# Kernel tuning notes

Hardware: AMD Instinct MI355X
Metric: run time of the kernel (lower is better)

## Reference

```python
import jax, jax.numpy as jnp
import numpy as np

B, C_IN, H, W = 32, 128, 64, 64
C_OUT, K, STRIDE, PAD = 128, 3, 1, 1
M, G = 2, 2
RC = max(C_IN // 16, 16)          # reduction channels = 16
MO = M * C_OUT                    # 256
GRP = G * C_OUT                   # fc groups = 256
OPG = (C_OUT * C_IN * K * K) // GRP   # 576 outputs per fc group
IPG = MO // GRP                   # 1 input per fc group
EPS = 1e-5


def setup_inputs() -> dict:
    key = jax.random.key(0)
    ks = jax.random.split(key, 12)
    s = 0.02
    return {
        "x": jax.random.normal(ks[0], (B, C_IN, H, W), jnp.float32),
        "mask_w": jax.random.normal(ks[1], (1, C_IN), jnp.float32) * s,
        "mask_b": jnp.zeros((1,), jnp.float32),
        "t1_w": jax.random.normal(ks[2], (RC, C_IN), jnp.float32) * s,
        "t1_b": jnp.zeros((RC,), jnp.float32),
        "ln_g": jnp.ones((RC,), jnp.float32),
        "ln_b": jnp.zeros((RC,), jnp.float32),
        "t2_w": jax.random.normal(ks[3], (MO, RC), jnp.float32) * s,
        "t2_b": jnp.zeros((MO,), jnp.float32),
        "fc_w": jax.random.normal(ks[4], (GRP, OPG, IPG), jnp.float32) * s,
        "fc_b": jnp.zeros((GRP * OPG,), jnp.float32),
    }


def reference(x, mask_w, mask_b, t1_w, t1_b, ln_g, ln_b, t2_w, t2_b, fc_w, fc_b):
    b, c, h, w = x.shape
    # --- GC attention context pooling ---
    logits = jnp.einsum('bchw,oc->bohw', x, mask_w) + mask_b[None, :, None, None]
    attn = jax.nn.softmax(logits.reshape(b, h * w), axis=-1)  # [b, hw]
    context = jnp.einsum('bchw,bs->bc', x, attn.reshape(b, h * w)) if False else \
        jnp.einsum('bcs,bs->bc', x.reshape(b, c, h * w), attn)
    # --- transform: conv1x1 -> LayerNorm -> ReLU -> conv1x1 ---
    t = jnp.einsum('bc,rc->br', context, t1_w) + t1_b
    mu = jnp.mean(t, axis=-1, keepdims=True)
    var = jnp.mean((t - mu) ** 2, axis=-1, keepdims=True)
    t = (t - mu) * jax.lax.rsqrt(var + EPS) * ln_g + ln_b
    t = jax.nn.relu(t)
    xw = jnp.einsum('br,or->bo', t, t2_w) + t2_b          # [b, M*out]
    xw = jax.nn.sigmoid(xw)
    # --- grouped 1x1 fc: generates per-sample conv weights ---
    xg = xw.reshape(b, GRP, IPG)
    gen = jnp.einsum('goi,bgi->bgo', fc_w, xg) + fc_b.reshape(GRP, OPG)
    w_gen = gen.reshape(b, C_OUT, C_IN, K, K)             # per-sample kernels
    # --- per-sample conv (groups=b trick in torch) ---
    def conv_one(xi, wi):
        return jax.lax.conv_general_dilated(
            xi[None], wi, (STRIDE, STRIDE), [(PAD, PAD), (PAD, PAD)],
            dimension_numbers=('NCHW', 'OIHW', 'NCHW'))[0]
    out = jax.vmap(conv_one)(x, w_gen)                    # [b, out, h, w]
    return out
```

## Files before the change

kernel.cpp:

```cpp
#include <hip/hip_runtime.h>
#include <hip/hip_bf16.h>

typedef unsigned short u16;
typedef unsigned int u32;
typedef __attribute__((ext_vector_type(8))) short bf16x8;
typedef __attribute__((ext_vector_type(16))) float f32x16;
typedef __attribute__((ext_vector_type(4))) int int4v;
typedef __attribute__((ext_vector_type(4))) float f32x4;

#define CIN 128
#define COUT 128
#define HWSZ 4096
#define RC 16
#define EPS 1e-5f

__device__ __forceinline__ float b2f(u16 u) {
    u32 v = ((u32)u) << 16;
    union { u32 i; float f; } c; c.i = v; return c.f;
}

__device__ __forceinline__ void dma16(const void* g, void* l) {
    __builtin_amdgcn_global_load_lds((const __attribute__((address_space(1))) void*)g,
                                     (__attribute__((address_space(3))) void*)l, 16, 0, 0);
}

__global__ __launch_bounds__(256) void k_xform(const float* __restrict__ x,
                                               const float* __restrict__ mask_w,
                                               const float* __restrict__ mask_b,
                                               u16* __restrict__ xT,
                                               float* __restrict__ attn,
                                               float* __restrict__ sumexp) {
    int y = blockIdx.x, b = blockIdx.y, t = threadIdx.x;
    __shared__ float tile[128 * 65];
    __shared__ float red[256];

    int c4 = t & 15, ci0 = t >> 4;
#pragma unroll
    for (int i = 0; i < 8; ++i) {
        int ci = ci0 + i * 16;
        f32x4 v = *(const f32x4*)(x + (size_t)(b * 128 + ci) * 4096 + y * 64 + c4 * 4);
        float* tr = tile + ci * 65 + c4 * 4;
        tr[0] = v.x; tr[1] = v.y; tr[2] = v.z; tr[3] = v.w;
    }
    __syncthreads();

    {
        int xs = t & 63, grp = t >> 6;
        float a = 0.f;
#pragma unroll 8
        for (int ci = grp * 32; ci < grp * 32 + 32; ++ci)
            a = fmaf(tile[ci * 65 + xs], mask_w[ci], a);
        red[grp * 64 + xs] = a;
    }

    {
        int xs = t >> 2, q = t & 3;
        u16* dst = xT + ((size_t)b * 4096 + y * 64 + xs) * 128;
        int sw = xs & 7;
#pragma unroll
        for (int k = 0; k < 4; ++k) {
            int cd = q * 4 + k;
            int cs = cd ^ sw;
            u16 tmp[8];
#pragma unroll
            for (int e = 0; e < 8; ++e) {
                __hip_bfloat16 h = __float2bfloat16(tile[(cd * 8 + e) * 65 + xs]);
                tmp[e] = *reinterpret_cast<u16*>(&h);
            }
            *(int4v*)(dst + cs * 8) = *(int4v*)tmp;
        }
    }
    __syncthreads();
    if (t < 64) {
        float e = __expf(red[t] + red[64 + t] + red[128 + t] + red[192 + t] + mask_b[0]);
        attn[b * HWSZ + y * 64 + t] = e;
        float s = e;
#pragma unroll
        for (int off = 32; off; off >>= 1) s += __shfl_down(s, off);
        if (t == 0) atomicAdd(&sumexp[b], s);
    }
}

__global__ __launch_bounds__(256) void k_context(const u16* __restrict__ xT,
                                                 const float* __restrict__ attn,
                                                 const float* __restrict__ sumexp,
                                                 float* __restrict__ ctx) {
    int bid = blockIdx.x;
    int b = bid >> 4, sc = bid & 15;
    int t = threadIdx.x;
    int px = t >> 4, cg = t & 15;
    const char* xb = (const char*)(xT + (size_t)b * HWSZ * 128);
    float acc[8] = {0.f, 0.f, 0.f, 0.f, 0.f, 0.f, 0.f, 0.f};
    int s0 = sc * 256 + px;
    int coff = (cg * 16) ^ ((px & 7) << 4);
    for (int j = 0; j < 16; ++j) {
        int s = s0 + j * 16;
        float e = attn[b * HWSZ + s];
        int4v u = *(const int4v*)(xb + (size_t)s * 256 + coff);
        const u16* q = (const u16*)&u;
#pragma unroll
        for (int k = 0; k < 8; ++k) acc[k] = fmaf(e, b2f(q[k]), acc[k]);
    }
    __shared__ float red[16][132];
#pragma unroll
    for (int k = 0; k < 8; ++k) red[px][cg * 8 + k] = acc[k];
    __syncthreads();
    if (t < 128) {
        float s = 0.f;
#pragma unroll
        for (int g = 0; g < 16; ++g) s += red[g][t];
        atomicAdd(&ctx[b * 128 + t], s / sumexp[b]);
    }
}

__global__ __launch_bounds__(256) void k_genw(const float* __restrict__ ctx,
                                              const float* __restrict__ t1_w,
                                              const float* __restrict__ t1_b,
                                              const float* __restrict__ ln_g,
                                              const float* __restrict__ ln_b,
                                              const float* __restrict__ t2_w,
                                              const float* __restrict__ t2_b,
                                              const float* __restrict__ fc_w,
                                              const float* __restrict__ fc_b,
                                              u16* __restrict__ wgen) {
    int bid = blockIdx.x;
    int b = bid >> 3, g = bid & 7;
    int t = threadIdx.x;
    __shared__ float ctx_sh[128];
    __shared__ float traw[RC];
    __shared__ float gate_sh[64];
    if (t < 128) ctx_sh[t] = ctx[b * 128 + t];
    __syncthreads();
    if (t < RC) {
        float a = 0.f;
        for (int c = 0; c < 128; ++c) a = fmaf(ctx_sh[c], t1_w[t * 128 + c], a);
        traw[t] = a + t1_b[t];
    }
    __syncthreads();
    int r32g = g >> 1;
    if (t < 64) {
        float tv[RC], mu = 0.f;
#pragma unroll
        for (int r = 0; r < RC; ++r) { tv[r] = traw[r]; mu += tv[r]; }
        mu *= (1.f / RC);
        float var = 0.f;
#pragma unroll
        for (int r = 0; r < RC; ++r) { float d = tv[r] - mu; var = fmaf(d, d, var); }
        var *= (1.f / RC);
        float rs = rsqrtf(var + EPS);
        int gi = r32g * 64 + t;
        float xw = 0.f;
#pragma unroll
        for (int r = 0; r < RC; ++r) {
            float a = fmaxf(0.f, fmaf((tv[r] - mu) * rs, ln_g[r], ln_b[r]));
            xw = fmaf(a, t2_w[gi * RC + r], xw);
        }
        xw += t2_b[gi];
        gate_sh[t] = 1.f / (1.f + __expf(-xw));
    }
    __syncthreads();
    int U = g * 256 + t;
    int r32 = U >> 9, c = (U >> 5) & 15, l31 = U & 31;
    int co = r32 * 32 + l31;
    float gate = gate_sh[l31 * 2 + (c >> 3)];
    int base = co * 1152 + c * 72;
    float wv[72], bv[72];
#pragma unroll
    for (int i = 0; i < 18; ++i) {
        *(f32x4*)&wv[i * 4] = *(const f32x4*)(fc_w + base + i * 4);
        *(f32x4*)&bv[i * 4] = *(const f32x4*)(fc_b + base + i * 4);
    }
    u16* wb = wgen + (size_t)b * 9 * 16384;
    int unit = r32 * 512 + c * 32 + l31;
#pragma unroll
    for (int p = 0; p < 9; ++p) {
        u16 tmp[8];
#pragma unroll
        for (int e = 0; e < 8; ++e) {
            float v = fmaf(wv[e * 9 + p], gate, bv[e * 9 + p]);
            __hip_bfloat16 h = __float2bfloat16(v);
            tmp[e] = *reinterpret_cast<u16*>(&h);
        }
        *(int4v*)(wb + p * 16384 + unit * 8) = *(int4v*)tmp;
    }
}

__global__ __launch_bounds__(256, 2) void k_conv(const u16* __restrict__ xT,
                                                 const u16* __restrict__ wgen,
                                                 float* __restrict__ out) {
    __shared__ __align__(16) u16 Bt[132 * 128];

    int bid0 = blockIdx.x;
    int xcd = bid0 & 7, i5 = bid0 >> 3;
    int b = xcd * 4 + (i5 >> 5);
    int yp = i5 & 31, y0 = yp * 2;

    int t = threadIdx.x;
    int lane = t & 63, w = t >> 6;
    int wr = w >> 1, wc = w & 1;
    int l31 = lane & 31, l5 = lane >> 5;

    const char* xb = (const char*)(xT + (size_t)b * HWSZ * 128);
    const char* wbase = (const char*)(wgen + (size_t)b * 9 * 16384);
    const char* abase = wbase + wr * 16384 + l5 * 512 + l31 * 16;

    bf16x8 RA[16], RB[16];
    f32x16 acc00 = {0}, acc01 = {0}, acc10 = {0}, acc11 = {0};
    const char* Bb = (const char*)Bt;
    int rowB0 = wc * 66 + l31;

#define LOADP(P, R)                                                        \
    {                                                                      \
        const char* ap = abase + (P) * 32768;                              \
        _Pragma("unroll") for (int ks = 0; ks < 8; ++ks) {                 \
            R[ks]     = *(const bf16x8*)(ap + ks * 1024);                  \
            R[8 + ks] = *(const bf16x8*)(ap + 8192 + ks * 1024);           \
        }                                                                  \
    }

#define COMPUTE(P, R)                                                              \
    {                                                                              \
        const int kw = (P) % 3;                                                    \
        int rB0 = (rowB0 + kw) << 8;                                               \
        int rB1 = rB0 + (32 << 8);                                                 \
        int sB = ((l31 + kw - 1) & 7) << 4;                                        \
        _Pragma("unroll") for (int ks = 0; ks < 8; ++ks) {                         \
            int kb = ks * 32 + l5 * 16;                                            \
            bf16x8 b0 = *(const bf16x8*)(Bb + (rB0 | (kb ^ sB)));                  \
            bf16x8 b1 = *(const bf16x8*)(Bb + (rB1 | (kb ^ sB)));                  \
            acc00 = __builtin_amdgcn_mfma_f32_32x32x16_bf16(R[ks], b0, acc00, 0, 0, 0);     \
            acc01 = __builtin_amdgcn_mfma_f32_32x32x16_bf16(R[ks], b1, acc01, 0, 0, 0);     \
            acc10 = __builtin_amdgcn_mfma_f32_32x32x16_bf16(R[8 + ks], b0, acc10, 0, 0, 0); \
            acc11 = __builtin_amdgcn_mfma_f32_32x32x16_bf16(R[8 + ks], b1, acc11, 0, 0, 0); \
        }                                                                          \
    }

#define STAGEB(KH)                                                                   \
    {                                                                                \
        _Pragma("unroll") for (int r = 0; r < 2; ++r) {                              \
            int y = y0 + r + (KH) - 1;                                               \
            char* base = (char*)Bt + (r * 66) * 256;                                 \
            if ((unsigned)y < 64u) {                                                 \
                const char* src = xb + (size_t)y * 64 * 256;                         \
                _Pragma("unroll") for (int i = 0; i < 4; ++i) {                      \
                    int off = (w * 4 + i) * 1024;                                    \
                    dma16(src + off + lane * 16, base + 256 + off);                  \
                }                                                                    \
                if (t < 32) {                                                        \
                    int hr = (t >> 4) * 65;                                          \
                    *(int4v*)(base + hr * 256 + (t & 15) * 16) = int4v{0, 0, 0, 0};  \
                }                                                                    \
            } else {                                                                 \
                for (int i = t; i < 1056; i += 256)                                  \
                    *(int4v*)(base + i * 16) = int4v{0, 0, 0, 0};                    \
            }                                                                        \
        }                                                                            \
    }

    LOADP(0, RA);
#pragma unroll
    for (int p = 0; p < 9; ++p) {
        if (p % 3 == 0) {
            __syncthreads();
            STAGEB(p / 3);
            __syncthreads();
        }
        if (p < 8) {
            if (p & 1) { LOADP(p + 1, RA); } else { LOADP(p + 1, RB); }
        }
        if (p & 1) { COMPUTE(p, RB); } else { COMPUTE(p, RA); }
    }

    float* ob = out + (size_t)b * COUT * HWSZ;
    int y = y0 + wc;
    auto store_acc = [&](const f32x16& v, int m2, int n4) {
        float* colp = ob + (size_t)(wr * 64 + m2 * 32) * HWSZ + y * 64 + n4 * 32 + l31;
#pragma unroll
        for (int r = 0; r < 16; ++r) {
            int row32 = (r & 3) + ((r >> 2) << 3) + (l5 << 2);
            colp[(size_t)row32 * HWSZ] = v[r];
        }
    };
    store_acc(acc00, 0, 0);
    store_acc(acc01, 0, 1);
    store_acc(acc10, 1, 0);
    store_acc(acc11, 1, 1);
#undef LOADP
#undef COMPUTE
#undef STAGEB
}

extern "C" void kernel_launch(void* const* d_in, const int* in_sizes, int n_in,
                              void* d_out, int out_size, void* d_ws, size_t ws_size,
                              hipStream_t stream) {
    const float* x      = (const float*)d_in[0];
    const float* mask_w = (const float*)d_in[1];
    const float* mask_b = (const float*)d_in[2];
    const float* t1_w   = (const float*)d_in[3];
    const float* t1_b   = (const float*)d_in[4];
    const float* ln_g   = (const float*)d_in[5];
    const float* ln_b   = (const float*)d_in[6];
    const float* t2_w   = (const float*)d_in[7];
    const float* t2_b   = (const float*)d_in[8];
    const float* fc_w   = (const float*)d_in[9];
    const float* fc_b   = (const float*)d_in[10];
    float* out = (float*)d_out;

    char* ws = (char*)d_ws;
    u16*   xT     = (u16*)ws;
    float* attn   = (float*)(ws + 33554432);
    float* ctx    = (float*)(ws + 34078720);
    float* sumexp = (float*)(ws + 34095104);
    u16*   wgen   = (u16*)(ws + 34096128);

    hipMemsetAsync(ws + 34078720, 0, 17408, stream);

    k_xform  <<<dim3(64, 32), 256, 0, stream>>>(x, mask_w, mask_b, xT, attn, sumexp);
    k_context<<<512, 256, 0, stream>>>(xT, attn, sumexp, ctx);
    k_genw   <<<256, 256, 0, stream>>>(ctx, t1_w, t1_b, ln_g, ln_b,
                                       t2_w, t2_b, fc_w, fc_b, wgen);
    k_conv   <<<1024, 256, 0, stream>>>(xT, wgen, out);
}
```

Baseline: 215.5 us.

## Fuse context pooling into transform kernel, re-grid weight generation, stage conv rows once

The attention-weighted context sum moves into k_xform. Each block computes unnormalized exp weights per row and accumulates e*x into the context buffer with atomics. This removes the separate k_context kernel and the attn buffer round trip. k_genw is re-gridded to 2048 blocks, with each thread producing one (co,ci) pair and writing scalar bf16 stores, and normalization by sumexp is deferred to it. k_conv stages all four input rows into LDS once up front instead of three synchronized restaging phases. This doubles its LDS use and may reduce occupancy.

Result: faster. 209.9 us (-2.6%).

```diff
diff --git a/kernel.cpp b/kernel.cpp
--- a/kernel.cpp
+++ b/kernel.cpp
@@ -14,11 +14,6 @@
 #define RC 16
 #define EPS 1e-5f
 
-__device__ __forceinline__ float b2f(u16 u) {
-    u32 v = ((u32)u) << 16;
-    union { u32 i; float f; } c; c.i = v; return c.f;
-}
-
 __device__ __forceinline__ void dma16(const void* g, void* l) {
     __builtin_amdgcn_global_load_lds((const __attribute__((address_space(1))) void*)g,
                                      (__attribute__((address_space(3))) void*)l, 16, 0, 0);
@@ -28,19 +23,19 @@
                                                const float* __restrict__ mask_w,
                                                const float* __restrict__ mask_b,
                                                u16* __restrict__ xT,
-                                               float* __restrict__ attn,
+                                               float* __restrict__ ctxU,
                                                float* __restrict__ sumexp) {
     int y = blockIdx.x, b = blockIdx.y, t = threadIdx.x;
-    __shared__ float tile[128 * 65];
+    __shared__ float tile[128 * 68];
     __shared__ float red[256];
+    __shared__ float e_sh[64];
 
     int c4 = t & 15, ci0 = t >> 4;
 #pragma unroll
     for (int i = 0; i < 8; ++i) {
         int ci = ci0 + i * 16;
         f32x4 v = *(const f32x4*)(x + (size_t)(b * 128 + ci) * 4096 + y * 64 + c4 * 4);
-        float* tr = tile + ci * 65 + c4 * 4;
-        tr[0] = v.x; tr[1] = v.y; tr[2] = v.z; tr[3] = v.w;
+        *(f32x4*)(tile + ci * 68 + c4 * 4) = v;
     }
     __syncthreads();
 
@@ -49,9 +44,19 @@
         float a = 0.f;
 #pragma unroll 8
         for (int ci = grp * 32; ci < grp * 32 + 32; ++ci)
-            a = fmaf(tile[ci * 65 + xs], mask_w[ci], a);
-        red[grp * 64 + xs] = a;
-    }
+            a = fmaf(tile[ci * 68 + xs], mask_w[ci], a);
+        red[t] = a;
+    }
+    __syncthreads();
+    if (t < 64) {
+        float e = __expf(red[t] + red[64 + t] + red[128 + t] + red[192 + t] + mask_b[0]);
+        e_sh[t] = e;
+        float s = e;
+#pragma unroll
+        for (int off = 32; off; off >>= 1) s += __shfl_down(s, off);
+        if (t == 0) atomicAdd(&sumexp[b], s);
+    }
+    __syncthreads();
 
     {
         int xs = t >> 2, q = t & 3;
@@ -63,57 +68,29 @@
             int cs = cd ^ sw;
             u16 tmp[8];
 #pragma unroll
-            for (int e = 0; e < 8; ++e) {
-                __hip_bfloat16 h = __float2bfloat16(tile[(cd * 8 + e) * 65 + xs]);
-                tmp[e] = *reinterpret_cast<u16*>(&h);
+            for (int e2 = 0; e2 < 8; ++e2) {
+                __hip_bfloat16 h = __float2bfloat16(tile[(cd * 8 + e2) * 68 + xs]);
+                tmp[e2] = *reinterpret_cast<u16*>(&h);
             }
             *(int4v*)(dst + cs * 8) = *(int4v*)tmp;
         }
     }
-    __syncthreads();
-    if (t < 64) {
-        float e = __expf(red[t] + red[64 + t] + red[128 + t] + red[192 + t] + mask_b[0]);
-        attn[b * HWSZ + y * 64 + t] = e;
-        float s = e;
-#pragma unroll
-        for (int off = 32; off; off >>= 1) s += __shfl_down(s, off);
-        if (t == 0) atomicAdd(&sumexp[b], s);
-    }
-}
-
-__global__ __launch_bounds__(256) void k_context(const u16* __restrict__ xT,
-                                                 const float* __restrict__ attn,
-                                                 const float* __restrict__ sumexp,
-                                                 float* __restrict__ ctx) {
-    int bid = blockIdx.x;
-    int b = bid >> 4, sc = bid & 15;
-    int t = threadIdx.x;
-    int px = t >> 4, cg = t & 15;
-    const char* xb = (const char*)(xT + (size_t)b * HWSZ * 128);
-    float acc[8] = {0.f, 0.f, 0.f, 0.f, 0.f, 0.f, 0.f, 0.f};
-    int s0 = sc * 256 + px;
-    int coff = (cg * 16) ^ ((px & 7) << 4);
-    for (int j = 0; j < 16; ++j) {
-        int s = s0 + j * 16;
-        float e = attn[b * HWSZ + s];
-        int4v u = *(const int4v*)(xb + (size_t)s * 256 + coff);
-        const u16* q = (const u16*)&u;
-#pragma unroll
-        for (int k = 0; k < 8; ++k) acc[k] = fmaf(e, b2f(q[k]), acc[k]);
-    }
-    __shared__ float red[16][132];
-#pragma unroll
-    for (int k = 0; k < 8; ++k) red[px][cg * 8 + k] = acc[k];
-    __syncthreads();
-    if (t < 128) {
-        float s = 0.f;
-#pragma unroll
-        for (int g = 0; g < 16; ++g) s += red[g][t];
-        atomicAdd(&ctx[b * 128 + t], s / sumexp[b]);
-    }
-}
-
-__global__ __launch_bounds__(256) void k_genw(const float* __restrict__ ctx,
+
+    {
+        int ci = t >> 1, half = t & 1;
+        float a = 0.f;
+#pragma unroll
+        for (int j = 0; j < 32; ++j) {
+            int xs = half * 32 + j;
+            a = fmaf(tile[ci * 68 + xs], e_sh[xs], a);
+        }
+        a += __shfl_xor(a, 1);
+        if (half == 0) atomicAdd(&ctxU[b * 128 + ci], a);
+    }
+}
+
+__global__ __launch_bounds__(256) void k_genw(const float* __restrict__ ctxU,
+                                              const float* __restrict__ sumexp,
                                               const float* __restrict__ t1_w,
                                               const float* __restrict__ t1_b,
                                               const float* __restrict__ ln_g,
@@ -124,12 +101,12 @@
                                               const float* __restrict__ fc_b,
                                               u16* __restrict__ wgen) {
     int bid = blockIdx.x;
-    int b = bid >> 3, g = bid & 7;
+    int b = bid >> 6, c64 = bid & 63;
     int t = threadIdx.x;
     __shared__ float ctx_sh[128];
     __shared__ float traw[RC];
-    __shared__ float gate_sh[64];
-    if (t < 128) ctx_sh[t] = ctx[b * 128 + t];
+    __shared__ float gate_sh[4];
+    if (t < 128) ctx_sh[t] = ctxU[b * 128 + t] / sumexp[b];
     __syncthreads();
     if (t < RC) {
         float a = 0.f;
@@ -137,8 +114,7 @@
         traw[t] = a + t1_b[t];
     }
     __syncthreads();
-    int r32g = g >> 1;
-    if (t < 64) {
+    if (t < 4) {
         float tv[RC], mu = 0.f;
 #pragma unroll
         for (int r = 0; r < RC; ++r) { tv[r] = traw[r]; mu += tv[r]; }
@@ -148,7 +124,7 @@
         for (int r = 0; r < RC; ++r) { float d = tv[r] - mu; var = fmaf(d, d, var); }
         var *= (1.f / RC);
         float rs = rsqrtf(var + EPS);
-        int gi = r32g * 64 + t;
+        int gi = (c64 * 2 + (t >> 1)) * 2 + (t & 1);
         float xw = 0.f;
 #pragma unroll
         for (int r = 0; r < RC; ++r) {
@@ -159,36 +135,26 @@
         gate_sh[t] = 1.f / (1.f + __expf(-xw));
     }
     __syncthreads();
-    int U = g * 256 + t;
-    int r32 = U >> 9, c = (U >> 5) & 15, l31 = U & 31;
-    int co = r32 * 32 + l31;
-    float gate = gate_sh[l31 * 2 + (c >> 3)];
-    int base = co * 1152 + c * 72;
-    float wv[72], bv[72];
-#pragma unroll
-    for (int i = 0; i < 18; ++i) {
-        *(f32x4*)&wv[i * 4] = *(const f32x4*)(fc_w + base + i * 4);
-        *(f32x4*)&bv[i * 4] = *(const f32x4*)(fc_b + base + i * 4);
-    }
+    int co = c64 * 2 + (t >> 7);
+    int ci = t & 127;
+    float gate = gate_sh[(t >> 7) * 2 + (ci >> 6)];
+    const float* wp = fc_w + co * 1152 + ci * 9;
+    const float* bp = fc_b + co * 1152 + ci * 9;
     u16* wb = wgen + (size_t)b * 9 * 16384;
-    int unit = r32 * 512 + c * 32 + l31;
+    int unit = (co >> 5) * 512 + (ci >> 3) * 32 + (co & 31);
+    u16* ubase = wb + unit * 8 + (ci & 7);
 #pragma unroll
     for (int p = 0; p < 9; ++p) {
-        u16 tmp[8];
-#pragma unroll
-        for (int e = 0; e < 8; ++e) {
-            float v = fmaf(wv[e * 9 + p], gate, bv[e * 9 + p]);
-            __hip_bfloat16 h = __float2bfloat16(v);
-            tmp[e] = *reinterpret_cast<u16*>(&h);
-        }
-        *(int4v*)(wb + p * 16384 + unit * 8) = *(int4v*)tmp;
+        float v = fmaf(wp[p], gate, bp[p]);
+        __hip_bfloat16 h = __float2bfloat16(v);
+        ubase[(size_t)p * 16384] = *reinterpret_cast<u16*>(&h);
     }
 }
 
 __global__ __launch_bounds__(256, 2) void k_conv(const u16* __restrict__ xT,
                                                  const u16* __restrict__ wgen,
                                                  float* __restrict__ out) {
-    __shared__ __align__(16) u16 Bt[132 * 128];
+    __shared__ __align__(16) u16 Bt[4 * 66 * 128];
 
     int bid0 = blockIdx.x;
     int xcd = bid0 & 7, i5 = bid0 >> 3;
@@ -206,8 +172,7 @@
 
     bf16x8 RA[16], RB[16];
     f32x16 acc00 = {0}, acc01 = {0}, acc10 = {0}, acc11 = {0};
-    const char* Bb = (const char*)Bt;
-    int rowB0 = wc * 66 + l31;
+    char* Bb = (char*)Bt;
 
 #define LOADP(P, R)                                                        \
     {                                                                      \
@@ -218,53 +183,49 @@
         }                                                                  \
     }
 
-#define COMPUTE(P, R)                                                              \
-    {                                                                              \
-        const int kw = (P) % 3;                                                    \
-        int rB0 = (rowB0 + kw) << 8;                                               \
-        int rB1 = rB0 + (32 << 8);                                                 \
-        int sB = ((l31 + kw - 1) & 7) << 4;                                        \
-        _Pragma("unroll") for (int ks = 0; ks < 8; ++ks) {                         \
-            int kb = ks * 32 + l5 * 16;                                            \
-            bf16x8 b0 = *(const bf16x8*)(Bb + (rB0 | (kb ^ sB)));                  \
-            bf16x8 b1 = *(const bf16x8*)(Bb + (rB1 | (kb ^ sB)));                  \
+#define COMPUTE(P, R)                                                               \
+    {                                                                               \
+        const int kw = (P) % 3;                                                     \
+        int rB0 = (wc + (P) / 3) * 16896 + (l31 + kw) * 256;                        \
+        int rB1 = rB0 + 8192;                                                       \
+        int sB = ((l31 + kw - 1) & 7) << 4;                                         \
+        _Pragma("unroll") for (int ks = 0; ks < 8; ++ks) {                          \
+            int kb = ks * 32 + l5 * 16;                                             \
+            bf16x8 b0 = *(const bf16x8*)(Bb + rB0 + (kb ^ sB));                     \
+            bf16x8 b1 = *(const bf16x8*)(Bb + rB1 + (kb ^ sB));                     \
             acc00 = __builtin_amdgcn_mfma_f32_32x32x16_bf16(R[ks], b0, acc00, 0, 0, 0);     \
             acc01 = __builtin_amdgcn_mfma_f32_32x32x16_bf16(R[ks], b1, acc01, 0, 0, 0);     \
             acc10 = __builtin_amdgcn_mfma_f32_32x32x16_bf16(R[8 + ks], b0, acc10, 0, 0, 0); \
             acc11 = __builtin_amdgcn_mfma_f32_32x32x16_bf16(R[8 + ks], b1, acc11, 0, 0, 0); \
-        }                                                                          \
-    }
-
-#define STAGEB(KH)                                                                   \
-    {                                                                                \
-        _Pragma("unroll") for (int r = 0; r < 2; ++r) {                              \
-            int y = y0 + r + (KH) - 1;                                               \
-            char* base = (char*)Bt + (r * 66) * 256;                                 \
-            if ((unsigned)y < 64u) {                                                 \
-                const char* src = xb + (size_t)y * 64 * 256;                         \
-                _Pragma("unroll") for (int i = 0; i < 4; ++i) {                      \
-                    int off = (w * 4 + i) * 1024;                                    \
-                    dma16(src + off + lane * 16, base + 256 + off);                  \
-                }                                                                    \
-                if (t < 32) {                                                        \
-                    int hr = (t >> 4) * 65;                                          \
-                    *(int4v*)(base + hr * 256 + (t & 15) * 16) = int4v{0, 0, 0, 0};  \
-                }                                                                    \
-            } else {                                                                 \
-                for (int i = t; i < 1056; i += 256)                                  \
-                    *(int4v*)(base + i * 16) = int4v{0, 0, 0, 0};                    \
-            }                                                                        \
-        }                                                                            \
+        }                                                                           \
     }
 
     LOADP(0, RA);
+
+#pragma unroll
+    for (int R = 0; R < 4; ++R) {
+        int y = y0 + R - 1;
+        char* base = Bb + R * 16896;
+        if ((unsigned)y < 64u) {
+            const char* src = xb + (size_t)y * 16384;
+#pragma unroll
+            for (int i = 0; i < 4; ++i) {
+                int off = (i * 256 + t) * 16;
+                dma16(src + off, base + 256 + off);
+            }
+        } else {
+            for (int i = t; i < 1056; i += 256)
+                *(int4v*)(base + i * 16) = int4v{0, 0, 0, 0};
+        }
+    }
+    if (t < 128) {
+        int R = t >> 5, side = (t >> 4) & 1, c = t & 15;
+        *(int4v*)(Bb + R * 16896 + side * 16640 + c * 16) = int4v{0, 0, 0, 0};
+    }
+    __syncthreads();
+
 #pragma unroll
     for (int p = 0; p < 9; ++p) {
-        if (p % 3 == 0) {
-            __syncthreads();
-            STAGEB(p / 3);
-            __syncthreads();
-        }
         if (p < 8) {
             if (p & 1) { LOADP(p + 1, RA); } else { LOADP(p + 1, RB); }
         }
@@ -287,7 +248,6 @@
     store_acc(acc11, 1, 1);
 #undef LOADP
 #undef COMPUTE
-#undef STAGEB
 }
 
 extern "C" void kernel_launch(void* const* d_in, const int* in_sizes, int n_in,
@@ -308,16 +268,14 @@
 
     char* ws = (char*)d_ws;
     u16*   xT     = (u16*)ws;
-    float* attn   = (float*)(ws + 33554432);
-    float* ctx    = (float*)(ws + 34078720);
-    float* sumexp = (float*)(ws + 34095104);
-    u16*   wgen   = (u16*)(ws + 34096128);
-
-    hipMemsetAsync(ws + 34078720, 0, 17408, stream);
-
-    k_xform  <<<dim3(64, 32), 256, 0, stream>>>(x, mask_w, mask_b, xT, attn, sumexp);
-    k_context<<<512, 256, 0, stream>>>(xT, attn, sumexp, ctx);
-    k_genw   <<<256, 256, 0, stream>>>(ctx, t1_w, t1_b, ln_g, ln_b,
-                                       t2_w, t2_b, fc_w, fc_b, wgen);
-    k_conv   <<<1024, 256, 0, stream>>>(xT, wgen, out);
-}
+    float* ctxU   = (float*)(ws + 33554432);
+    float* sumexp = (float*)(ws + 33570816);
+    u16*   wgen   = (u16*)(ws + 33571840);
+
+    hipMemsetAsync(ws + 33554432, 0, 17408, stream);
+
+    k_xform<<<dim3(64, 32), 256, 0, stream>>>(x, mask_w, mask_b, xT, ctxU, sumexp);
+    k_genw <<<2048, 256, 0, stream>>>(ctxU, sumexp, t1_w, t1_b, ln_g, ln_b,
+                                      t2_w, t2_b, fc_w, fc_b, wgen);
+    k_conv <<<1024, 256, 0, stream>>>(xT, wgen, out);
+}
```
